# Kernel tuning notes

Measured on AMD Instinct MI355X. Metric: run time of the kernel, lower is better.

Reference implementation:

```python
import jax, jax.numpy as jnp
from jax import lax
import numpy as np

B, T, I, H, C = 2048, 512, 46, 64, 8

def setup_inputs() -> dict:
    key = jax.random.key(0)
    ks = jax.random.split(key, 7)
    s_ih = 1.0 / np.sqrt(H)  # PyTorch GRU init scale ~ U(-1/sqrt(H), 1/sqrt(H)); use scaled normal
    return {
        "x": jax.random.normal(ks[0], (B, T, I), jnp.float32),
        "w_ih": jax.random.normal(ks[1], (3 * H, I), jnp.float32) * s_ih,
        "w_hh": jax.random.normal(ks[2], (3 * H, H), jnp.float32) * s_ih,
        "b_ih": jax.random.normal(ks[3], (3 * H,), jnp.float32) * s_ih,
        "b_hh": jax.random.normal(ks[4], (3 * H,), jnp.float32) * s_ih,
        "fc_w": jax.random.normal(ks[5], (C, H), jnp.float32) * (1.0 / np.sqrt(H)),
        "fc_b": jax.random.normal(ks[6], (C,), jnp.float32) * (1.0 / np.sqrt(H)),
    }

def reference(x, w_ih, w_hh, b_ih, b_hh, fc_w, fc_b):
    # x: [B, T, I]. PyTorch GRU gate order: r, z, n.
    Bv, Tv, _ = x.shape
    Hv = w_hh.shape[1]
    # Precompute input contributions for all timesteps: [B, T, 3H]
    gx = jnp.einsum('bti,gi->btg', x, w_ih) + b_ih
    gx_t = jnp.swapaxes(gx, 0, 1)  # [T, B, 3H] for scan

    def step(h, gxt):
        gh = h @ w_hh.T + b_hh  # [B, 3H]
        xr, xz, xn = jnp.split(gxt, 3, axis=-1)
        hr, hz, hn = jnp.split(gh, 3, axis=-1)
        r = jax.nn.sigmoid(xr + hr)
        z = jax.nn.sigmoid(xz + hz)
        n = jnp.tanh(xn + r * hn)
        h_new = (1.0 - z) * n + z * h
        return h_new, None

    h0 = jnp.zeros((Bv, Hv), x.dtype)
    h_last, _ = lax.scan(step, h0, gx_t)  # last hidden == output[:, -1, :]
    logits = h_last @ fc_w.T + fc_b  # [B, C]
    return jax.nn.softmax(logits, axis=1)
```

## Files before the change

### kernel.cpp

```cpp
#include <hip/hip_runtime.h>
#include <hip/hip_bf16.h>

#define TT 512
#define II 46
#define HH 64
#define GG 192
#define CC 8
#define RR 8

typedef __attribute__((ext_vector_type(8))) _Float16 half8;
typedef __attribute__((ext_vector_type(4))) float float4v;

__device__ inline float fsigm(float xv) {
  return __builtin_amdgcn_rcpf(1.f + __expf(-xv));
}
__device__ inline float ftanh2(float xv) {
  float e = __expf(2.f * xv);
  float uu = __builtin_amdgcn_rcpf(1.f + e);
  return __builtin_fmaf(-2.f, uu, 1.f);
}

__global__ void pack_w(const float* __restrict__ w_ih, const float* __restrict__ w_hh,
                       _Float16* __restrict__ wph, _Float16* __restrict__ wpx) {
  int idx = blockIdx.x * 256 + threadIdx.x;
  if (idx < GG * HH) {
    wph[idx] = (_Float16)w_hh[idx];
  } else {
    idx -= GG * HH;
    if (idx < GG * 64) {
      int g = idx >> 6, k = idx & 63;
      wpx[idx] = (_Float16)(k < II ? w_ih[g * II + k] : 0.f);
    }
  }
}

__launch_bounds__(512, 2)
__global__ void gru_main(const float* __restrict__ x,
                         const float* __restrict__ b_ih, const float* __restrict__ b_hh,
                         const float* __restrict__ fc_w, const float* __restrict__ fc_b,
                         const _Float16* __restrict__ wph,
                         const _Float16* __restrict__ wpx,
                         float* __restrict__ out) {
  __shared__ __align__(16) _Float16 hsf[2][2][64][8];
  __shared__ __align__(16) _Float16 xsf[2][2][64][8];
  __shared__ __align__(16) float gxpT[2][3][64][12];
  __shared__ float hf[RR][HH + 1];
  __shared__ float fcw[CC * HH];
  __shared__ float fcbs[CC];
  __shared__ float lgts[RR][CC];

  const int tau = threadIdx.x;
  const int w8  = tau >> 6;
  const int l   = tau & 63;
  const int m16 = l & 15;
  const int kg  = l >> 4;
  const int row0 = blockIdx.x * RR;

  {
    _Float16* hz = &hsf[0][0][0][0];
    for (int i = tau; i < 2 * 2 * 64 * 8; i += 512) hz[i] = (_Float16)0.f;
    _Float16* xz = &xsf[0][0][0][0];
    for (int i = tau; i < 2 * 2 * 64 * 8; i += 512) xz[i] = (_Float16)0.f;
  }
  __syncthreads();

  float hreg[2] = {0.f, 0.f};
  const int row0l = (kg & 1) * 4 + ((kg >> 1) & 1) * 2;

  if (w8 < 4) {
    const int u = 16 * w8 + m16;
    const float bnh = b_hh[128 + u];
    half8 bh[3][2];
    {
      const int gbs[3] = {16 * w8, 64 + 16 * w8, 128 + 16 * w8};
#pragma unroll
      for (int tt = 0; tt < 3; ++tt) {
        const _Float16* bb = wph + (size_t)(gbs[tt] + m16) * 64 + kg * 8;
        bh[tt][0] = *(const half8*)(bb);
        bh[tt][1] = *(const half8*)(bb + 32);
      }
    }
    const int sh  = w8 >> 1;
    const int kgp = (u >> 3) & 3;
    const int jp  = u & 7;
    const bool lo2 = (kg < 2);

    __syncthreads();
    __builtin_amdgcn_s_setprio(1);

    for (int t = 0; t < TT; ++t) {
      __syncthreads();
      const int cur = t & 1, nxt = cur ^ 1;
      half8 a0 = *(const half8*)&hsf[cur][0][l][0];
      half8 a1 = *(const half8*)&hsf[cur][1][l][0];
      float2 gR = *(const float2*)&gxpT[cur][0][u][row0l];
      float2 gZ = *(const float2*)&gxpT[cur][1][u][row0l];
      float2 gN = *(const float2*)&gxpT[cur][2][u][row0l];

      float4v accr = {0.f, 0.f, 0.f, 0.f};
      float4v accz = {0.f, 0.f, 0.f, 0.f};
      float4v accn = {bnh, bnh, bnh, bnh};
      accr = __builtin_amdgcn_mfma_f32_16x16x32_f16(a0, bh[0][0], accr, 0, 0, 0);
      accz = __builtin_amdgcn_mfma_f32_16x16x32_f16(a0, bh[1][0], accz, 0, 0, 0);
      accn = __builtin_amdgcn_mfma_f32_16x16x32_f16(a0, bh[2][0], accn, 0, 0, 0);
      accr = __builtin_amdgcn_mfma_f32_16x16x32_f16(a1, bh[0][1], accr, 0, 0, 0);
      accz = __builtin_amdgcn_mfma_f32_16x16x32_f16(a1, bh[1][1], accz, 0, 0, 0);
      accn = __builtin_amdgcn_mfma_f32_16x16x32_f16(a1, bh[2][1], accn, 0, 0, 0);

      float r2 = __shfl_xor(accr[2], 32), r3 = __shfl_xor(accr[3], 32);
      float z2 = __shfl_xor(accz[2], 32), z3 = __shfl_xor(accz[3], 32);
      float n2 = __shfl_xor(accn[2], 32), n3 = __shfl_xor(accn[3], 32);
      float aR[2] = {lo2 ? accr[0] : r2, lo2 ? accr[1] : r3};
      float aZ[2] = {lo2 ? accz[0] : z2, lo2 ? accz[1] : z3};
      float aN[2] = {lo2 ? accn[0] : n2, lo2 ? accn[1] : n3};
      float gr[2] = {gR.x, gR.y}, gz[2] = {gZ.x, gZ.y}, gn[2] = {gN.x, gN.y};

#pragma unroll
      for (int i = 0; i < 2; ++i) {
        float rg = fsigm(aR[i] + gr[i]);
        float zg = fsigm(aZ[i] + gz[i]);
        float pre = __builtin_fmaf(rg, aN[i], gn[i]);
        float ng = ftanh2(pre);
        hreg[i] = ng + zg * (hreg[i] - ng);
        hsf[nxt][sh][kgp * 16 + row0l + i][jp] = (_Float16)hreg[i];
      }
    }
    __builtin_amdgcn_s_setprio(0);
  } else {
    const int wp = w8 - 4;
    const int u = 16 * wp + m16;
    const float br = b_ih[u] + b_hh[u];
    const float bz = b_ih[64 + u] + b_hh[64 + u];
    const float bn = b_ih[128 + u];
    half8 bx[3][2];
    {
      const int gbs[3] = {16 * wp, 64 + 16 * wp, 128 + 16 * wp};
#pragma unroll
      for (int tt = 0; tt < 3; ++tt) {
        const _Float16* bb = wpx + (size_t)(gbs[tt] + m16) * 64 + kg * 8;
        bx[tt][0] = *(const half8*)(bb);
        bx[tt][1] = *(const half8*)(bb + 32);
      }
    }
    const bool wr = (kg < 2);

    const int p = tau - 256;
    const int r1 = p / II, i1 = p % II;
    const bool has2 = (p + 256) < RR * II;
    const int e2 = p + 256;
    const int r2g = has2 ? (e2 / II) : r1;
    const int i2g = has2 ? (e2 % II) : i1;
    const float* xp1 = x + (size_t)(row0 + r1) * TT * II + i1;
    const float* xp2 = x + (size_t)(row0 + r2g) * TT * II + i2g;
    const int s1 = i1 >> 5, kg1 = (i1 >> 3) & 3, j1 = i1 & 7;
    const int s2 = i2g >> 5, kg2 = (i2g >> 3) & 3, j2 = i2g & 7;

    auto stageX = [&](int buf, float va, float vb) {
      xsf[buf][s1][kg1 * 16 + r1][j1] = (_Float16)va;
      if (has2) xsf[buf][s2][kg2 * 16 + r2g][j2] = (_Float16)vb;
    };
    auto produceGx = [&](int buf) {
      half8 a0 = *(const half8*)&xsf[buf][0][l][0];
      half8 a1 = *(const half8*)&xsf[buf][1][l][0];
      float4v ar = {br, br, br, br};
      float4v az = {bz, bz, bz, bz};
      float4v an = {bn, bn, bn, bn};
      ar = __builtin_amdgcn_mfma_f32_16x16x32_f16(a0, bx[0][0], ar, 0, 0, 0);
      az = __builtin_amdgcn_mfma_f32_16x16x32_f16(a0, bx[1][0], az, 0, 0, 0);
      an = __builtin_amdgcn_mfma_f32_16x16x32_f16(a0, bx[2][0], an, 0, 0, 0);
      ar = __builtin_amdgcn_mfma_f32_16x16x32_f16(a1, bx[0][1], ar, 0, 0, 0);
      az = __builtin_amdgcn_mfma_f32_16x16x32_f16(a1, bx[1][1], az, 0, 0, 0);
      an = __builtin_amdgcn_mfma_f32_16x16x32_f16(a1, bx[2][1], an, 0, 0, 0);
      if (wr) {
        *(float4v*)&gxpT[buf][0][u][kg * 4] = ar;
        *(float4v*)&gxpT[buf][1][u][kg * 4] = az;
        *(float4v*)&gxpT[buf][2][u][kg * 4] = an;
      }
    };

    float v0a = xp1[0], v0b = xp2[0];
    float v1a = xp1[II], v1b = xp2[II];
    float xc1 = xp1[2 * II], xc2 = xp2[2 * II];
    stageX(0, v0a, v0b);
    __syncthreads();
    produceGx(0);
    stageX(1, v1a, v1b);

    for (int t = 0; t < TT; ++t) {
      __syncthreads();
      float nx1 = 0.f, nx2 = 0.f;
      if (t + 3 < TT) {
        nx1 = xp1[(size_t)(t + 3) * II];
        nx2 = xp2[(size_t)(t + 3) * II];
      }
      if (t + 1 < TT) produceGx((t + 1) & 1);
      if (t + 2 < TT) stageX(t & 1, xc1, xc2);
      xc1 = nx1; xc2 = nx2;
    }
  }

  if (w8 < 4) {
    hf[row0l + 0][16 * w8 + m16] = hreg[0];
    hf[row0l + 1][16 * w8 + m16] = hreg[1];
  }
  fcw[tau] = fc_w[tau];
  if (tau < CC) fcbs[tau] = fc_b[tau];
  __syncthreads();
  if (tau < RR * CC) {
    int rr = tau >> 3, c = tau & 7;
    float acc = fcbs[c];
#pragma unroll
    for (int j = 0; j < HH; ++j) acc += hf[rr][j] * fcw[c * HH + j];
    lgts[rr][c] = acc;
  }
  __syncthreads();
  if (tau < RR * CC) {
    int rr = tau >> 3, c = tau & 7;
    float mx = lgts[rr][0];
#pragma unroll
    for (int j = 1; j < CC; ++j) mx = fmaxf(mx, lgts[rr][j]);
    float ssum = 0.f;
#pragma unroll
    for (int j = 0; j < CC; ++j) ssum += __expf(lgts[rr][j] - mx);
    out[(size_t)(row0 + rr) * CC + c] = __expf(lgts[rr][c] - mx) / ssum;
  }
}

extern "C" void kernel_launch(void* const* d_in, const int* in_sizes, int n_in,
                              void* d_out, int out_size, void* d_ws, size_t ws_size,
                              hipStream_t stream) {
  const float* x    = (const float*)d_in[0];
  const float* w_ih = (const float*)d_in[1];
  const float* w_hh = (const float*)d_in[2];
  const float* b_ih = (const float*)d_in[3];
  const float* b_hh = (const float*)d_in[4];
  const float* fc_w = (const float*)d_in[5];
  const float* fc_b = (const float*)d_in[6];

  _Float16* wph = (_Float16*)d_ws;
  _Float16* wpx = wph + GG * HH;

  pack_w<<<96, 256, 0, stream>>>(w_ih, w_hh, wph, wpx);
  gru_main<<<256, 512, 0, stream>>>(x, b_ih, b_hh, fc_w, fc_b, wph, wpx, (float*)d_out);
}
```

Before: 200.7 us.

## Fuse input projection into recurrent MFMA step with concatenated K=128 weights

Removes the producer/consumer warp specialization, where four waves computed the input-gate projection into shared memory a step ahead for four recurrent waves. Each wave now runs one concatenated MFMA over [h; x] against packed [w_hh | w_ih] weights, with a separate n-gate split into hidden and input parts. This drops the gxpT shared buffer and its extra LDS traffic, and halves the block to 256 threads. The trade-off is that the x projection now sits on the serial critical path of every timestep instead of overlapping with it, and there are fewer waves to hide latency.

Result: slower. 255.4 us (+27.3%).

```diff
diff --git a/kernel.cpp b/kernel.cpp
--- a/kernel.cpp
+++ b/kernel.cpp
@@ -7,6 +7,7 @@
 #define GG 192
 #define CC 8
 #define RR 8
+#define KP 128
 
 typedef __attribute__((ext_vector_type(8))) _Float16 half8;
 typedef __attribute__((ext_vector_type(4))) float float4v;
@@ -16,194 +17,143 @@
 }
 __device__ inline float ftanh2(float xv) {
   float e = __expf(2.f * xv);
-  float uu = __builtin_amdgcn_rcpf(1.f + e);
-  return __builtin_fmaf(-2.f, uu, 1.f);
+  return __builtin_fmaf(-2.f, __builtin_amdgcn_rcpf(1.f + e), 1.f);
 }
 
 __global__ void pack_w(const float* __restrict__ w_ih, const float* __restrict__ w_hh,
-                       _Float16* __restrict__ wph, _Float16* __restrict__ wpx) {
+                       _Float16* __restrict__ wp) {
   int idx = blockIdx.x * 256 + threadIdx.x;
-  if (idx < GG * HH) {
-    wph[idx] = (_Float16)w_hh[idx];
-  } else {
-    idx -= GG * HH;
-    if (idx < GG * 64) {
-      int g = idx >> 6, k = idx & 63;
-      wpx[idx] = (_Float16)(k < II ? w_ih[g * II + k] : 0.f);
-    }
-  }
+  int u = idx >> 7, k = idx & 127;
+  float v = (k < HH) ? w_hh[u * HH + k]
+                     : ((k < HH + II) ? w_ih[u * II + (k - HH)] : 0.f);
+  wp[idx] = (_Float16)v;
 }
 
-__launch_bounds__(512, 2)
+__launch_bounds__(256, 1)
 __global__ void gru_main(const float* __restrict__ x,
                          const float* __restrict__ b_ih, const float* __restrict__ b_hh,
                          const float* __restrict__ fc_w, const float* __restrict__ fc_b,
-                         const _Float16* __restrict__ wph,
-                         const _Float16* __restrict__ wpx,
+                         const _Float16* __restrict__ wp,
                          float* __restrict__ out) {
   __shared__ __align__(16) _Float16 hsf[2][2][64][8];
   __shared__ __align__(16) _Float16 xsf[2][2][64][8];
-  __shared__ __align__(16) float gxpT[2][3][64][12];
   __shared__ float hf[RR][HH + 1];
   __shared__ float fcw[CC * HH];
   __shared__ float fcbs[CC];
   __shared__ float lgts[RR][CC];
 
   const int tau = threadIdx.x;
-  const int w8  = tau >> 6;
+  const int w4  = tau >> 6;
   const int l   = tau & 63;
   const int m16 = l & 15;
   const int kg  = l >> 4;
   const int row0 = blockIdx.x * RR;
 
   {
-    _Float16* hz = &hsf[0][0][0][0];
-    for (int i = tau; i < 2 * 2 * 64 * 8; i += 512) hz[i] = (_Float16)0.f;
-    _Float16* xz = &xsf[0][0][0][0];
-    for (int i = tau; i < 2 * 2 * 64 * 8; i += 512) xz[i] = (_Float16)0.f;
+    _Float16* p = &hsf[0][0][0][0];
+    for (int i = tau; i < 2 * 2 * 64 * 8; i += 256) p[i] = (_Float16)0.f;
+    p = &xsf[0][0][0][0];
+    for (int i = tau; i < 2 * 2 * 64 * 8; i += 256) p[i] = (_Float16)0.f;
   }
-  __syncthreads();
+
+  const int u = 16 * w4 + m16;
+  const float br  = b_ih[u] + b_hh[u];
+  const float bz  = b_ih[64 + u] + b_hh[64 + u];
+  const float bnx = b_ih[128 + u];
+  const float bnh = b_hh[128 + u];
+
+  half8 bf[3][4];
+#pragma unroll
+  for (int g = 0; g < 3; ++g) {
+    const _Float16* bb = wp + (size_t)(64 * g + u) * KP + kg * 8;
+#pragma unroll
+    for (int s = 0; s < 4; ++s) bf[g][s] = *(const half8*)(bb + 32 * s);
+  }
+
+  const int sh  = w4 >> 1;
+  const int kgp = (u >> 3) & 3;
+  const int jp  = u & 7;
+  const int row0l = (kg & 1) * 4 + (kg >> 1) * 2;
+  const bool lo2 = (kg < 2);
+
+  const int r1 = tau / II, i1 = tau % II;
+  const bool has2 = (tau + 256) < RR * II;
+  const int e2 = tau + 256;
+  const int r2 = has2 ? e2 / II : r1, i2 = has2 ? e2 % II : i1;
+  const float* xp1 = x + (size_t)(row0 + r1) * TT * II + i1;
+  const float* xp2 = x + (size_t)(row0 + r2) * TT * II + i2;
+  const int s1 = i1 >> 5, kg1 = (i1 >> 3) & 3, j1 = i1 & 7;
+  const int s2 = i2 >> 5, kg2 = (i2 >> 3) & 3, j2 = i2 & 7;
+
+  auto stageX = [&](int buf, float va, float vb) {
+    xsf[buf][s1][kg1 * 16 + r1][j1] = (_Float16)va;
+    if (has2) xsf[buf][s2][kg2 * 16 + r2][j2] = (_Float16)vb;
+  };
 
   float hreg[2] = {0.f, 0.f};
-  const int row0l = (kg & 1) * 4 + ((kg >> 1) & 1) * 2;
 
-  if (w8 < 4) {
-    const int u = 16 * w8 + m16;
-    const float bnh = b_hh[128 + u];
-    half8 bh[3][2];
-    {
-      const int gbs[3] = {16 * w8, 64 + 16 * w8, 128 + 16 * w8};
-#pragma unroll
-      for (int tt = 0; tt < 3; ++tt) {
-        const _Float16* bb = wph + (size_t)(gbs[tt] + m16) * 64 + kg * 8;
-        bh[tt][0] = *(const half8*)(bb);
-        bh[tt][1] = *(const half8*)(bb + 32);
-      }
+  float v0a = xp1[0],       v0b = has2 ? xp2[0] : 0.f;
+  float xc1 = xp1[II],      xc2 = has2 ? xp2[II] : 0.f;
+  float xn1 = xp1[2 * II],  xn2 = has2 ? xp2[2 * II] : 0.f;
+  __syncthreads();
+  stageX(0, v0a, v0b);
+
+  for (int t = 0; t < TT; ++t) {
+    __syncthreads();
+    const int cur = t & 1, nxt = cur ^ 1;
+    half8 a0 = *(const half8*)&hsf[cur][0][l][0];
+    half8 a1 = *(const half8*)&hsf[cur][1][l][0];
+    half8 a2 = *(const half8*)&xsf[cur][0][l][0];
+    half8 a3 = *(const half8*)&xsf[cur][1][l][0];
+
+    float4v accr  = {br, br, br, br};
+    float4v accz  = {bz, bz, bz, bz};
+    float4v accnh = {bnh, bnh, bnh, bnh};
+    float4v accnx = {bnx, bnx, bnx, bnx};
+    accr  = __builtin_amdgcn_mfma_f32_16x16x32_f16(a0, bf[0][0], accr, 0, 0, 0);
+    accr  = __builtin_amdgcn_mfma_f32_16x16x32_f16(a1, bf[0][1], accr, 0, 0, 0);
+    accr  = __builtin_amdgcn_mfma_f32_16x16x32_f16(a2, bf[0][2], accr, 0, 0, 0);
+    accr  = __builtin_amdgcn_mfma_f32_16x16x32_f16(a3, bf[0][3], accr, 0, 0, 0);
+    accz  = __builtin_amdgcn_mfma_f32_16x16x32_f16(a0, bf[1][0], accz, 0, 0, 0);
+    accz  = __builtin_amdgcn_mfma_f32_16x16x32_f16(a1, bf[1][1], accz, 0, 0, 0);
+    accz  = __builtin_amdgcn_mfma_f32_16x16x32_f16(a2, bf[1][2], accz, 0, 0, 0);
+    accz  = __builtin_amdgcn_mfma_f32_16x16x32_f16(a3, bf[1][3], accz, 0, 0, 0);
+    accnh = __builtin_amdgcn_mfma_f32_16x16x32_f16(a0, bf[2][0], accnh, 0, 0, 0);
+    accnh = __builtin_amdgcn_mfma_f32_16x16x32_f16(a1, bf[2][1], accnh, 0, 0, 0);
+    accnx = __builtin_amdgcn_mfma_f32_16x16x32_f16(a2, bf[2][2], accnx, 0, 0, 0);
+    accnx = __builtin_amdgcn_mfma_f32_16x16x32_f16(a3, bf[2][3], accnx, 0, 0, 0);
+
+    if (t + 1 < TT) stageX(nxt, xc1, xc2);
+    xc1 = xn1; xc2 = xn2;
+    if (t + 3 < TT) {
+      xn1 = xp1[(size_t)(t + 3) * II];
+      if (has2) xn2 = xp2[(size_t)(t + 3) * II];
     }
-    const int sh  = w8 >> 1;
-    const int kgp = (u >> 3) & 3;
-    const int jp  = u & 7;
-    const bool lo2 = (kg < 2);
 
-    __syncthreads();
-    __builtin_amdgcn_s_setprio(1);
-
-    for (int t = 0; t < TT; ++t) {
-      __syncthreads();
-      const int cur = t & 1, nxt = cur ^ 1;
-      half8 a0 = *(const half8*)&hsf[cur][0][l][0];
-      half8 a1 = *(const half8*)&hsf[cur][1][l][0];
-      float2 gR = *(const float2*)&gxpT[cur][0][u][row0l];
-      float2 gZ = *(const float2*)&gxpT[cur][1][u][row0l];
-      float2 gN = *(const float2*)&gxpT[cur][2][u][row0l];
-
-      float4v accr = {0.f, 0.f, 0.f, 0.f};
-      float4v accz = {0.f, 0.f, 0.f, 0.f};
-      float4v accn = {bnh, bnh, bnh, bnh};
-      accr = __builtin_amdgcn_mfma_f32_16x16x32_f16(a0, bh[0][0], accr, 0, 0, 0);
-      accz = __builtin_amdgcn_mfma_f32_16x16x32_f16(a0, bh[1][0], accz, 0, 0, 0);
-      accn = __builtin_amdgcn_mfma_f32_16x16x32_f16(a0, bh[2][0], accn, 0, 0, 0);
-      accr = __builtin_amdgcn_mfma_f32_16x16x32_f16(a1, bh[0][1], accr, 0, 0, 0);
-      accz = __builtin_amdgcn_mfma_f32_16x16x32_f16(a1, bh[1][1], accz, 0, 0, 0);
-      accn = __builtin_amdgcn_mfma_f32_16x16x32_f16(a1, bh[2][1], accn, 0, 0, 0);
-
-      float r2 = __shfl_xor(accr[2], 32), r3 = __shfl_xor(accr[3], 32);
-      float z2 = __shfl_xor(accz[2], 32), z3 = __shfl_xor(accz[3], 32);
-      float n2 = __shfl_xor(accn[2], 32), n3 = __shfl_xor(accn[3], 32);
-      float aR[2] = {lo2 ? accr[0] : r2, lo2 ? accr[1] : r3};
-      float aZ[2] = {lo2 ? accz[0] : z2, lo2 ? accz[1] : z3};
-      float aN[2] = {lo2 ? accn[0] : n2, lo2 ? accn[1] : n3};
-      float gr[2] = {gR.x, gR.y}, gz[2] = {gZ.x, gZ.y}, gn[2] = {gN.x, gN.y};
+    float r2s = __shfl_xor(accr[2], 32),  r3s = __shfl_xor(accr[3], 32);
+    float z2s = __shfl_xor(accz[2], 32),  z3s = __shfl_xor(accz[3], 32);
+    float h2s = __shfl_xor(accnh[2], 32), h3s = __shfl_xor(accnh[3], 32);
+    float x2s = __shfl_xor(accnx[2], 32), x3s = __shfl_xor(accnx[3], 32);
+    float aR[2]  = {lo2 ? accr[0]  : r2s, lo2 ? accr[1]  : r3s};
+    float aZ[2]  = {lo2 ? accz[0]  : z2s, lo2 ? accz[1]  : z3s};
+    float aNH[2] = {lo2 ? accnh[0] : h2s, lo2 ? accnh[1] : h3s};
+    float aNX[2] = {lo2 ? accnx[0] : x2s, lo2 ? accnx[1] : x3s};
 
 #pragma unroll
-      for (int i = 0; i < 2; ++i) {
-        float rg = fsigm(aR[i] + gr[i]);
-        float zg = fsigm(aZ[i] + gz[i]);
-        float pre = __builtin_fmaf(rg, aN[i], gn[i]);
-        float ng = ftanh2(pre);
-        hreg[i] = ng + zg * (hreg[i] - ng);
-        hsf[nxt][sh][kgp * 16 + row0l + i][jp] = (_Float16)hreg[i];
-      }
-    }
-    __builtin_amdgcn_s_setprio(0);
-  } else {
-    const int wp = w8 - 4;
-    const int u = 16 * wp + m16;
-    const float br = b_ih[u] + b_hh[u];
-    const float bz = b_ih[64 + u] + b_hh[64 + u];
-    const float bn = b_ih[128 + u];
-    half8 bx[3][2];
-    {
-      const int gbs[3] = {16 * wp, 64 + 16 * wp, 128 + 16 * wp};
-#pragma unroll
-      for (int tt = 0; tt < 3; ++tt) {
-        const _Float16* bb = wpx + (size_t)(gbs[tt] + m16) * 64 + kg * 8;
-        bx[tt][0] = *(const half8*)(bb);
-        bx[tt][1] = *(const half8*)(bb + 32);
-      }
-    }
-    const bool wr = (kg < 2);
-
-    const int p = tau - 256;
-    const int r1 = p / II, i1 = p % II;
-    const bool has2 = (p + 256) < RR * II;
-    const int e2 = p + 256;
-    const int r2g = has2 ? (e2 / II) : r1;
-    const int i2g = has2 ? (e2 % II) : i1;
-    const float* xp1 = x + (size_t)(row0 + r1) * TT * II + i1;
-    const float* xp2 = x + (size_t)(row0 + r2g) * TT * II + i2g;
-    const int s1 = i1 >> 5, kg1 = (i1 >> 3) & 3, j1 = i1 & 7;
-    const int s2 = i2g >> 5, kg2 = (i2g >> 3) & 3, j2 = i2g & 7;
-
-    auto stageX = [&](int buf, float va, float vb) {
-      xsf[buf][s1][kg1 * 16 + r1][j1] = (_Float16)va;
-      if (has2) xsf[buf][s2][kg2 * 16 + r2g][j2] = (_Float16)vb;
-    };
-    auto produceGx = [&](int buf) {
-      half8 a0 = *(const half8*)&xsf[buf][0][l][0];
-      half8 a1 = *(const half8*)&xsf[buf][1][l][0];
-      float4v ar = {br, br, br, br};
-      float4v az = {bz, bz, bz, bz};
-      float4v an = {bn, bn, bn, bn};
-      ar = __builtin_amdgcn_mfma_f32_16x16x32_f16(a0, bx[0][0], ar, 0, 0, 0);
-      az = __builtin_amdgcn_mfma_f32_16x16x32_f16(a0, bx[1][0], az, 0, 0, 0);
-      an = __builtin_amdgcn_mfma_f32_16x16x32_f16(a0, bx[2][0], an, 0, 0, 0);
-      ar = __builtin_amdgcn_mfma_f32_16x16x32_f16(a1, bx[0][1], ar, 0, 0, 0);
-      az = __builtin_amdgcn_mfma_f32_16x16x32_f16(a1, bx[1][1], az, 0, 0, 0);
-      an = __builtin_amdgcn_mfma_f32_16x16x32_f16(a1, bx[2][1], an, 0, 0, 0);
-      if (wr) {
-        *(float4v*)&gxpT[buf][0][u][kg * 4] = ar;
-        *(float4v*)&gxpT[buf][1][u][kg * 4] = az;
-        *(float4v*)&gxpT[buf][2][u][kg * 4] = an;
-      }
-    };
-
-    float v0a = xp1[0], v0b = xp2[0];
-    float v1a = xp1[II], v1b = xp2[II];
-    float xc1 = xp1[2 * II], xc2 = xp2[2 * II];
-    stageX(0, v0a, v0b);
-    __syncthreads();
-    produceGx(0);
-    stageX(1, v1a, v1b);
-
-    for (int t = 0; t < TT; ++t) {
-      __syncthreads();
-      float nx1 = 0.f, nx2 = 0.f;
-      if (t + 3 < TT) {
-        nx1 = xp1[(size_t)(t + 3) * II];
-        nx2 = xp2[(size_t)(t + 3) * II];
-      }
-      if (t + 1 < TT) produceGx((t + 1) & 1);
-      if (t + 2 < TT) stageX(t & 1, xc1, xc2);
-      xc1 = nx1; xc2 = nx2;
+    for (int i = 0; i < 2; ++i) {
+      float rg = fsigm(aR[i]);
+      float zg = fsigm(aZ[i]);
+      float pre = __builtin_fmaf(rg, aNH[i], aNX[i]);
+      float ng = ftanh2(pre);
+      hreg[i] = ng + zg * (hreg[i] - ng);
+      hsf[nxt][sh][kgp * 16 + row0l + i][jp] = (_Float16)hreg[i];
     }
   }
 
-  if (w8 < 4) {
-    hf[row0l + 0][16 * w8 + m16] = hreg[0];
-    hf[row0l + 1][16 * w8 + m16] = hreg[1];
-  }
+  hf[row0l + 0][u] = hreg[0];
+  hf[row0l + 1][u] = hreg[1];
   fcw[tau] = fc_w[tau];
+  fcw[tau + 256] = fc_w[tau + 256];
   if (tau < CC) fcbs[tau] = fc_b[tau];
   __syncthreads();
   if (tau < RR * CC) {
@@ -237,9 +187,8 @@
   const float* fc_w = (const float*)d_in[5];
   const float* fc_b = (const float*)d_in[6];
 
-  _Float16* wph = (_Float16*)d_ws;
-  _Float16* wpx = wph + GG * HH;
+  _Float16* wp = (_Float16*)d_ws;
 
-  pack_w<<<96, 256, 0, stream>>>(w_ih, w_hh, wph, wpx);
-  gru_main<<<256, 512, 0, stream>>>(x, b_ih, b_hh, fc_w, fc_b, wph, wpx, (float*)d_out);
+  pack_w<<<96, 256, 0, stream>>>(w_ih, w_hh, wp);
+  gru_main<<<256, 256, 0, stream>>>(x, b_ih, b_hh, fc_w, fc_b, wp, (float*)d_out);
 }
```
